# Kernel tuning notes

Hardware: AMD Instinct MI355X
Metric: run time of the kernel (lower is better)

The kernel has to match this reference:

```python
import jax, jax.numpy as jnp
import numpy as np

NUM_REGIONS = 32   # region labels are 1..NUM_REGIONS, 0 = background
EPS = 1e-8


def setup_inputs() -> dict:
    key = jax.random.key(0)
    k1, k2 = jax.random.split(key)
    B, D, H, W = 4, 160, 192, 192
    x = jax.random.normal(k1, (B, 1, D, H, W), dtype=jnp.float32)
    # precomputed connected-component label map (0 = background)
    region_map = jax.random.randint(k2, (B, D, H, W), 0, NUM_REGIONS + 1, dtype=jnp.int32)
    return {"x": x, "region_map": region_map}


def _per_volume_sums(xf, seg):
    # xf: [V] sigmoid probs, seg: [V] region ids in [0, NUM_REGIONS]
    xs = jax.ops.segment_sum(xf, seg, num_segments=NUM_REGIONS + 1)
    cnt = jax.ops.segment_sum(jnp.ones_like(xf), seg, num_segments=NUM_REGIONS + 1)
    return xs, cnt


def reference(x, region_map):
    B = x.shape[0]
    probs = jax.nn.sigmoid(x)                      # x.dim()==5 -> sigmoid
    xf = probs.reshape(B, -1)                      # [B, V]
    seg = region_map.reshape(B, -1)                # [B, V]
    xs, cnt = jax.vmap(_per_volume_sums)(xf, seg)  # [B, R+1] each
    xs_r = xs[:, 1:]                               # per-region sum of sigmoid(x)
    cnt_r = cnt[:, 1:]                             # per-region voxel count (= sum of binary y)
    # dice over the region: y==1 inside the region, so intersection == xs_r
    dice = 2.0 * xs_r / (xs_r + cnt_r + EPS)       # [B, R]
    valid = cnt_r > 0                              # region actually present
    n_valid = jnp.sum(valid, axis=-1)              # [B]
    mean_dice = jnp.sum(jnp.where(valid, dice, 0.0), axis=-1) / jnp.maximum(n_valid, 1)
    loss_b = jnp.where(n_valid > 0, 1.0 - mean_dice, 1.0)  # num_features==0 -> loss 1.0
    return jnp.mean(loss_b)
```

## Files before the change

kernel.cpp:

```cpp
#include <hip/hip_runtime.h>

#define NUM_REGIONS 32
#define NBINS 33
#define BATCH 4
#define DHW (160*192*192)
#define NVEC_PER_BATCH (DHW/4)
#define BLOCKS_PER_BATCH 384
#define NBLOCKS (BATCH*BLOCKS_PER_BATCH)
#define VEC_PER_BLOCK (NVEC_PER_BATCH/BLOCKS_PER_BATCH)
#define ITERS (VEC_PER_BLOCK/256)
#define COL_STRIDE 129
#define EPS 1e-8f

__global__ __launch_bounds__(256) void region_sums_kernel(
    const float* __restrict__ x,
    const int*   __restrict__ seg,
    float*       __restrict__ ws)
{
    __shared__ float hist[NBINS * COL_STRIDE];
    __shared__ float part_xs [8][NBINS];
    __shared__ float part_cnt[8][NBINS];

    const int tid = threadIdx.x;
    const int col = tid >> 1;

    for (int i = tid; i < NBINS * COL_STRIDE; i += 256) hist[i] = 0.0f;
    __syncthreads();

    const int batch = blockIdx.x / BLOCKS_PER_BATCH;
    const int local = blockIdx.x - batch * BLOCKS_PER_BATCH;
    const int vbase = batch * NVEC_PER_BATCH + local * VEC_PER_BLOCK + tid;

    const float4* __restrict__ xv4 = (const float4*)x;
    const int4*   __restrict__ sv4 = (const int4*)seg;

    float4 xA = xv4[vbase];       int4 sA = sv4[vbase];
    float4 xB = xv4[vbase + 256]; int4 sB = sv4[vbase + 256];

    for (int k = 0; k < ITERS; ++k) {
        int kn = (k + 2 < ITERS) ? (k + 2) : (ITERS - 1);
        float4 xN = xv4[vbase + kn * 256];
        int4   sN = sv4[vbase + kn * 256];

        float p0 = __fdividef(1.0f, 1.0f + __expf(-xA.x)) + 256.0f;
        float p1 = __fdividef(1.0f, 1.0f + __expf(-xA.y)) + 256.0f;
        float p2 = __fdividef(1.0f, 1.0f + __expf(-xA.z)) + 256.0f;
        float p3 = __fdividef(1.0f, 1.0f + __expf(-xA.w)) + 256.0f;

        atomicAdd(&hist[sA.x * COL_STRIDE + col], p0);
        atomicAdd(&hist[sA.y * COL_STRIDE + col], p1);
        atomicAdd(&hist[sA.z * COL_STRIDE + col], p2);
        atomicAdd(&hist[sA.w * COL_STRIDE + col], p3);

        xA = xB; sA = sB; xB = xN; sB = sN;
    }
    __syncthreads();

    {
        const int bin = (tid & 31) + 1;
        const int g   = tid >> 5;
        float xs = 0.0f, cnt = 0.0f;
        #pragma unroll
        for (int j = 0; j < 16; ++j) {
            float V = hist[bin * COL_STRIDE + g * 16 + j];
            float c = floorf(V * (1.0f / 256.0f));
            cnt += c;
            xs  += V - 256.0f * c;
        }
        part_xs [g][bin] = xs;
        part_cnt[g][bin] = cnt;
    }
    __syncthreads();

    if (tid < 32) {
        const int bin = tid + 1;
        float xs = 0.0f, cnt = 0.0f;
        #pragma unroll
        for (int g = 0; g < 8; ++g) {
            xs  += part_xs [g][bin];
            cnt += part_cnt[g][bin];
        }
        atomicAdd(&ws[batch * NBINS + bin], xs);
        atomicAdd(&ws[BATCH * NBINS + batch * NBINS + bin], cnt);
    }
}

__global__ void region_dice_final_kernel(
    const float* __restrict__ ws,
    float*       __restrict__ out)
{
    const int lane = threadIdx.x;
    float loss_sum = 0.0f;

    for (int b = 0; b < BATCH; ++b) {
        bool  valid = false;
        float dice  = 0.0f;
        if (lane >= 1 && lane <= NUM_REGIONS) {
            float xs  = ws[b * NBINS + lane];
            float cnt = ws[BATCH * NBINS + b * NBINS + lane];
            valid = (cnt > 0.0f);
            if (valid) dice = 2.0f * xs / (xs + cnt + EPS);
        }
        unsigned long long m = __ballot(valid);
        int n_valid = __popcll(m);

        float s = dice;
        #pragma unroll
        for (int off = 32; off >= 1; off >>= 1) s += __shfl_down(s, off);

        float mean_dice = s / (float)((n_valid > 1) ? n_valid : 1);
        float loss_b    = (n_valid > 0) ? (1.0f - mean_dice) : 1.0f;
        loss_sum += loss_b;
    }

    if (lane == 0) out[0] = loss_sum * (1.0f / BATCH);
}

extern "C" void kernel_launch(void* const* d_in, const int* in_sizes, int n_in,
                              void* d_out, int out_size, void* d_ws, size_t ws_size,
                              hipStream_t stream)
{
    const float* x   = (const float*)d_in[0];
    const int*   seg = (const int*)d_in[1];
    float*       ws  = (float*)d_ws;

    hipMemsetAsync(d_ws, 0, 2 * BATCH * NBINS * sizeof(float), stream);

    region_sums_kernel<<<NBLOCKS, 256, 0, stream>>>(x, seg, ws);
    region_dice_final_kernel<<<1, 64, 0, stream>>>(ws, (float*)d_out);
}
```

Baseline: 262.6 us.

## Replace shared-memory atomic histogram with per-thread register bin accumulators

Each thread now keeps 32 register accumulators, one per region. Every element's sigmoid value, packed together with its count, is added into the matching bin through a compare-and-select chain, which removes all LDS atomics from the hot loop. The accumulators are written to shared memory once at the end for the block reduction. Blocks per batch drop from 384 to 256, and a tail pass handles the remainder. This trades atomic contention for about 32 compare-select-add steps per element and higher register pressure.

```diff
diff --git a/kernel.cpp b/kernel.cpp
--- a/kernel.cpp
+++ b/kernel.cpp
@@ -5,65 +5,88 @@
 #define BATCH 4
 #define DHW (160*192*192)
 #define NVEC_PER_BATCH (DHW/4)
-#define BLOCKS_PER_BATCH 384
+#define BLOCKS_PER_BATCH 256
 #define NBLOCKS (BATCH*BLOCKS_PER_BATCH)
 #define VEC_PER_BLOCK (NVEC_PER_BATCH/BLOCKS_PER_BATCH)
-#define ITERS (VEC_PER_BLOCK/256)
-#define COL_STRIDE 129
+#define FULL_ITERS (VEC_PER_BLOCK/256)
+#define TAIL_START (FULL_ITERS*256)
+#define RED_STRIDE 257
 #define EPS 1e-8f
 
-__global__ __launch_bounds__(256) void region_sums_kernel(
+__global__ __launch_bounds__(256, 4) void region_sums_kernel(
     const float* __restrict__ x,
     const int*   __restrict__ seg,
     float*       __restrict__ ws)
 {
-    __shared__ float hist[NBINS * COL_STRIDE];
-    __shared__ float part_xs [8][NBINS];
-    __shared__ float part_cnt[8][NBINS];
+    __shared__ float red[32 * RED_STRIDE];
+    __shared__ float part_xs [8][32];
+    __shared__ float part_cnt[8][32];
 
-    const int tid = threadIdx.x;
-    const int col = tid >> 1;
+    float acc[32];
+    #pragma unroll
+    for (int b = 0; b < 32; ++b) acc[b] = 0.0f;
 
-    for (int i = tid; i < NBINS * COL_STRIDE; i += 256) hist[i] = 0.0f;
-    __syncthreads();
-
-    const int batch = blockIdx.x / BLOCKS_PER_BATCH;
-    const int local = blockIdx.x - batch * BLOCKS_PER_BATCH;
-    const int vbase = batch * NVEC_PER_BATCH + local * VEC_PER_BLOCK + tid;
+    const int tid   = threadIdx.x;
+    const int batch = blockIdx.x >> 8;
+    const int local = blockIdx.x & 255;
+    const int vbase = batch * NVEC_PER_BATCH + local * VEC_PER_BLOCK;
 
     const float4* __restrict__ xv4 = (const float4*)x;
     const int4*   __restrict__ sv4 = (const int4*)seg;
 
-    float4 xA = xv4[vbase];       int4 sA = sv4[vbase];
-    float4 xB = xv4[vbase + 256]; int4 sB = sv4[vbase + 256];
+    float4 xA = xv4[vbase + tid];       int4 sA = sv4[vbase + tid];
+    float4 xB = xv4[vbase + tid + 256]; int4 sB = sv4[vbase + tid + 256];
 
-    for (int k = 0; k < ITERS; ++k) {
-        int kn = (k + 2 < ITERS) ? (k + 2) : (ITERS - 1);
-        float4 xN = xv4[vbase + kn * 256];
-        int4   sN = sv4[vbase + kn * 256];
+    #pragma unroll 1
+    for (int k = 0; k < FULL_ITERS; ++k) {
+        const int kn = (k + 2 < FULL_ITERS) ? (k + 2) : (FULL_ITERS - 1);
+        float4 xN = xv4[vbase + kn * 256 + tid];
+        int4   sN = sv4[vbase + kn * 256 + tid];
 
         float p0 = __fdividef(1.0f, 1.0f + __expf(-xA.x)) + 256.0f;
         float p1 = __fdividef(1.0f, 1.0f + __expf(-xA.y)) + 256.0f;
         float p2 = __fdividef(1.0f, 1.0f + __expf(-xA.z)) + 256.0f;
         float p3 = __fdividef(1.0f, 1.0f + __expf(-xA.w)) + 256.0f;
 
-        atomicAdd(&hist[sA.x * COL_STRIDE + col], p0);
-        atomicAdd(&hist[sA.y * COL_STRIDE + col], p1);
-        atomicAdd(&hist[sA.z * COL_STRIDE + col], p2);
-        atomicAdd(&hist[sA.w * COL_STRIDE + col], p3);
+        #pragma unroll
+        for (int b = 0; b < 32; ++b) {
+            acc[b] += (sA.x == b + 1) ? p0 : 0.0f;
+            acc[b] += (sA.y == b + 1) ? p1 : 0.0f;
+            acc[b] += (sA.z == b + 1) ? p2 : 0.0f;
+            acc[b] += (sA.w == b + 1) ? p3 : 0.0f;
+        }
 
         xA = xB; sA = sB; xB = xN; sB = sN;
     }
+
+    if (tid < VEC_PER_BLOCK - TAIL_START) {
+        float4 xT = xv4[vbase + TAIL_START + tid];
+        int4   sT = sv4[vbase + TAIL_START + tid];
+        float p0 = __fdividef(1.0f, 1.0f + __expf(-xT.x)) + 256.0f;
+        float p1 = __fdividef(1.0f, 1.0f + __expf(-xT.y)) + 256.0f;
+        float p2 = __fdividef(1.0f, 1.0f + __expf(-xT.z)) + 256.0f;
+        float p3 = __fdividef(1.0f, 1.0f + __expf(-xT.w)) + 256.0f;
+        #pragma unroll
+        for (int b = 0; b < 32; ++b) {
+            acc[b] += (sT.x == b + 1) ? p0 : 0.0f;
+            acc[b] += (sT.y == b + 1) ? p1 : 0.0f;
+            acc[b] += (sT.z == b + 1) ? p2 : 0.0f;
+            acc[b] += (sT.w == b + 1) ? p3 : 0.0f;
+        }
+    }
+
+    #pragma unroll
+    for (int b = 0; b < 32; ++b) red[b * RED_STRIDE + tid] = acc[b];
     __syncthreads();
 
     {
-        const int bin = (tid & 31) + 1;
+        const int bin = tid & 31;
         const int g   = tid >> 5;
         float xs = 0.0f, cnt = 0.0f;
         #pragma unroll
-        for (int j = 0; j < 16; ++j) {
-            float V = hist[bin * COL_STRIDE + g * 16 + j];
-            float c = floorf(V * (1.0f / 256.0f));
+        for (int j = 0; j < 32; ++j) {
+            float V = red[bin * RED_STRIDE + g * 32 + j];
+            float c = truncf(V * (1.0f / 256.0f));
             cnt += c;
             xs  += V - 256.0f * c;
         }
@@ -73,15 +96,14 @@
     __syncthreads();
 
     if (tid < 32) {
-        const int bin = tid + 1;
         float xs = 0.0f, cnt = 0.0f;
         #pragma unroll
         for (int g = 0; g < 8; ++g) {
-            xs  += part_xs [g][bin];
-            cnt += part_cnt[g][bin];
+            xs  += part_xs [g][tid];
+            cnt += part_cnt[g][tid];
         }
-        atomicAdd(&ws[batch * NBINS + bin], xs);
-        atomicAdd(&ws[BATCH * NBINS + batch * NBINS + bin], cnt);
+        atomicAdd(&ws[batch * NBINS + tid + 1], xs);
+        atomicAdd(&ws[BATCH * NBINS + batch * NBINS + tid + 1], cnt);
     }
 }
 
```

After: 218.8 us. 16.7% less time.
